# Kernel tuning notes

Hardware: AMD Instinct MI355X
Metric: run time of the kernel (lower is better)

## Reference

```python
import jax, jax.numpy as jnp
import numpy as np

D_MODEL = 1024
HIDDEN = 2816
N_EXPERTS = 8
N_ACTIVE = 2
THRESH = 1.0  # snntorch Leaky default threshold; single-step spike = (input > 1.0)


def setup_inputs() -> dict:
    key = jax.random.key(0)
    ks = jax.random.split(key, 10)
    s = 0.02
    return {
        "x": jax.random.normal(ks[0], (2, 1024, D_MODEL), jnp.float32),
        "Wg": jax.random.normal(ks[1], (D_MODEL, N_EXPERTS), jnp.float32) * s,
        "bg": jnp.zeros((N_EXPERTS,), jnp.float32),
        "W_gate": jax.random.normal(ks[2], (N_EXPERTS, D_MODEL, HIDDEN), jnp.float32) * s,
        "b_gate": jnp.zeros((N_EXPERTS, HIDDEN), jnp.float32),
        "W_up": jax.random.normal(ks[3], (N_EXPERTS, D_MODEL, HIDDEN), jnp.float32) * s,
        "b_up": jnp.zeros((N_EXPERTS, HIDDEN), jnp.float32),
        "W_down": jax.random.normal(ks[4], (N_EXPERTS, HIDDEN, D_MODEL), jnp.float32) * s,
        "b_down": jnp.zeros((N_EXPERTS, D_MODEL), jnp.float32),
    }


def reference(x, Wg, bg, W_gate, b_gate, W_up, b_up, W_down, b_down):
    B, S, D = x.shape
    xf = x.reshape(-1, D)  # [T, D]
    # spiking gate: single-step Leaky => spike = heaviside(logits - 1.0)
    gate_logits = xf @ Wg + bg  # [T, E]
    spike_out = (gate_logits > THRESH).astype(x.dtype)
    top_v, top_idx = jax.lax.top_k(spike_out, N_ACTIVE)  # [T, K]
    top_w = jax.nn.softmax(top_v, axis=-1)  # [T, K]
    # combine weights per expert: sum_k onehot(idx_k) * w_k  -> [T, E]
    combine = jnp.sum(jax.nn.one_hot(top_idx, N_EXPERTS, dtype=x.dtype) * top_w[..., None], axis=1)
    # per-expert SpikingSwiGLU: spike(gate_proj(x)) * up_proj(x) -> down_proj
    g = jnp.einsum("td,edh->teh", xf, W_gate) + b_gate  # [T, E, H]
    u = jnp.einsum("td,edh->teh", xf, W_up) + b_up
    h = (g > THRESH).astype(x.dtype) * u
    y = jnp.einsum("teh,ehd->ted", h, W_down) + b_down  # [T, E, D]
    out = jnp.einsum("ted,te->td", y, combine)
    return out.reshape(B, S, D)
```

## Files before the change

### kernel.cpp

```cpp
#include <hip/hip_runtime.h>


#define D_MODEL 1024
#define HID     2816
#define NEXP    8
#define NTOK    2048
#define NPAIR   4096
#define TM      128
#define MAXTILES 40
#define FLAGCAP  65536
#define KC      384
#define BAND    3e-4f
#define INNER   2e-5

typedef short s8v __attribute__((ext_vector_type(8)));
typedef float f4v __attribute__((ext_vector_type(4)));

__device__ __forceinline__ unsigned short f2bf(float f) {
  unsigned u = __float_as_uint(f);
  u += 0x7FFFu + ((u >> 16) & 1u);
  return (unsigned short)(u >> 16);
}
__device__ __forceinline__ float bf2f(unsigned short s) {
  return __uint_as_float(((unsigned)s) << 16);
}

__device__ __forceinline__ void gld16(const unsigned short* g, unsigned short* l) {
  __builtin_amdgcn_global_load_lds(
      (const __attribute__((address_space(1))) void*)g,
      (__attribute__((address_space(3))) void*)l, 16, 0, 0);
}

__device__ __forceinline__ bool np_spike(const float* __restrict__ xr,
                                         const float* __restrict__ wcol,
                                         size_t stride, float bias) {
  float g = 0.0f;
  for (int p0 = 0; p0 < D_MODEL; p0 += KC) {
    const int pe = min(p0 + KC, D_MODEL);
    float s = 0.0f;
    for (int d = p0; d < pe; ++d)
      s = fmaf(xr[d], wcol[(size_t)d * stride], s);
    g += s;
  }
  g += bias;
  return g > 1.0f;
}

__global__ void k_convx(const float* __restrict__ x, unsigned short* __restrict__ xh,
                        unsigned short* __restrict__ xl) {
  const int i = blockIdx.x * 256 + threadIdx.x;
  const float4 v = ((const float4*)x)[i];
  ushort4 h, l;
  h.x = f2bf(v.x); l.x = f2bf(v.x - bf2f(h.x));
  h.y = f2bf(v.y); l.y = f2bf(v.y - bf2f(h.y));
  h.z = f2bf(v.z); l.z = f2bf(v.z - bf2f(h.z));
  h.w = f2bf(v.w); l.w = f2bf(v.w - bf2f(h.w));
  ((ushort4*)xh)[i] = h;
  ((ushort4*)xl)[i] = l;
}

__global__ void k_convw(const float* __restrict__ in, unsigned short* __restrict__ hi,
                        unsigned short* __restrict__ lo, int R, int C) {
  const int e = blockIdx.y;
  const int ntx = C >> 6;
  const int tx = blockIdx.x % ntx;
  const int ty = blockIdx.x / ntx;
  const float* src = in + (size_t)e * R * C;
  const size_t obase = (size_t)e * R * C;
  __shared__ float t[64][65];
  const int tid = threadIdx.x;
#pragma unroll
  for (int it = 0; it < 4; ++it) {
    const int r = it * 16 + (tid >> 4);
    const float4 v = *(const float4*)(src + (size_t)(ty * 64 + r) * C + tx * 64 + (tid & 15) * 4);
    t[r][(tid & 15) * 4 + 0] = v.x;
    t[r][(tid & 15) * 4 + 1] = v.y;
    t[r][(tid & 15) * 4 + 2] = v.z;
    t[r][(tid & 15) * 4 + 3] = v.w;
  }
  __syncthreads();
#pragma unroll
  for (int it = 0; it < 2; ++it) {
    const int c = it * 32 + (tid >> 3);
    const int d0 = (tid & 7) * 8;
    s8v vh, vl;
#pragma unroll
    for (int i = 0; i < 8; ++i) {
      const float f = t[d0 + i][c];
      const unsigned short h = f2bf(f);
      vh[i] = (short)h;
      vl[i] = (short)f2bf(f - bf2f(h));
    }
    const size_t o = obase + (size_t)(tx * 64 + c) * R + ty * 64 + d0;
    *(s8v*)(hi + o) = vh;
    if (lo) *(s8v*)(lo + o) = vl;
  }
}

__global__ void k_router(const float* __restrict__ x, const float* __restrict__ Wg,
                         const float* __restrict__ bg, int* __restrict__ top_e,
                         float* __restrict__ top_w) {
  const int t = (blockIdx.x * blockDim.x + threadIdx.x) >> 6;
  const int lane = threadIdx.x & 63;
  if (t >= NTOK) return;
  const float* xr = x + (size_t)t * D_MODEL;
  double acc[NEXP];
#pragma unroll
  for (int e = 0; e < NEXP; ++e) acc[e] = 0.0;
#pragma unroll
  for (int i = 0; i < D_MODEL / 64; ++i) {
    const int d = lane + 64 * i;
    const double xv = (double)xr[d];
    const float4 w0 = *(const float4*)(Wg + d * NEXP);
    const float4 w1 = *(const float4*)(Wg + d * NEXP + 4);
    acc[0] = fma(xv, (double)w0.x, acc[0]);
    acc[1] = fma(xv, (double)w0.y, acc[1]);
    acc[2] = fma(xv, (double)w0.z, acc[2]);
    acc[3] = fma(xv, (double)w0.w, acc[3]);
    acc[4] = fma(xv, (double)w1.x, acc[4]);
    acc[5] = fma(xv, (double)w1.y, acc[5]);
    acc[6] = fma(xv, (double)w1.z, acc[6]);
    acc[7] = fma(xv, (double)w1.w, acc[7]);
  }
#pragma unroll
  for (int e = 0; e < NEXP; ++e) {
#pragma unroll
    for (int s = 32; s > 0; s >>= 1) acc[e] += __shfl_down(acc[e], s);
  }
  if (lane == 0) {
    bool sp[NEXP];
#pragma unroll
    for (int e = 0; e < NEXP; ++e) {
      const double l = acc[e] + (double)bg[e];
      if (fabs(l - 1.0) < INNER)
        sp[e] = np_spike(xr, Wg + e, NEXP, bg[e]);
      else
        sp[e] = l > 1.0;
    }
    int e0 = -1, e1 = -1;
    for (int e = 0; e < NEXP; ++e) if (sp[e])  { if (e0 < 0) e0 = e; else if (e1 < 0) e1 = e; }
    for (int e = 0; e < NEXP; ++e) if (!sp[e]) { if (e0 < 0) e0 = e; else if (e1 < 0) e1 = e; }
    float w0v, w1v;
    if (sp[e0] == sp[e1]) { w0v = 0.5f; w1v = 0.5f; }
    else { w0v = 0.7310585786300049f; w1v = 0.2689414213699951f; }
    top_e[2 * t] = e0; top_e[2 * t + 1] = e1;
    top_w[2 * t] = w0v; top_w[2 * t + 1] = w1v;
  }
}

__global__ void k_group(const int* __restrict__ top_e,
                        int* __restrict__ pair_token, int* __restrict__ pair_expert,
                        int* __restrict__ tok_pair, int4* __restrict__ tile_tab,
                        int* __restrict__ meta) {
  __shared__ int cnt[NEXP], off[NEXP + 1], fill[NEXP];
  const int tid = threadIdx.x;
  if (tid < NEXP) { cnt[tid] = 0; fill[tid] = 0; }
  __syncthreads();
  for (int i = tid; i < NPAIR; i += 256) atomicAdd(&cnt[top_e[i]], 1);
  __syncthreads();
  if (tid == 0) {
    off[0] = 0;
    for (int e = 0; e < NEXP; ++e) off[e + 1] = off[e] + cnt[e];
    int nt = 0;
    for (int e = 0; e < NEXP; ++e)
      for (int s = 0; s < cnt[e]; s += TM) {
        tile_tab[nt] = make_int4(e, off[e] + s, min(TM, cnt[e] - s), 0);
        ++nt;
      }
    meta[0] = nt;
    meta[1] = 0;
  }
  __syncthreads();
  for (int i = tid; i < NPAIR; i += 256) {
    const int e = top_e[i];
    const int pos = off[e] + atomicAdd(&fill[e], 1);
    pair_token[pos] = i >> 1;
    pair_expert[pos] = e;
    tok_pair[i] = pos;
  }
}

__launch_bounds__(256, 2)
__global__ void k_stage_a_bf(const unsigned short* __restrict__ xh,
                             const unsigned short* __restrict__ xl,
                             const unsigned short* __restrict__ wgh,
                             const unsigned short* __restrict__ wgl,
                             const unsigned short* __restrict__ wuh,
                             const float* __restrict__ bgate, const float* __restrict__ bup,
                             const int* __restrict__ pair_token,
                             const int4* __restrict__ tile_tab,
                             int* meta,
                             unsigned short* __restrict__ hbuf,
                             unsigned int* __restrict__ flags) {
  const int NB = HID / 128;
  const int tile_id = blockIdx.x / NB;
  const int bn = blockIdx.x % NB;
  if (tile_id >= meta[0]) return;
  const int4 tt = tile_tab[tile_id];
  const int e = tt.x, row0 = tt.y, rows = tt.z;
  const int n0 = bn * 128;

  __shared__ __align__(16) unsigned short lds[5 * 4096];

  const int tid = threadIdx.x;
  const int lane = tid & 63;
  const int wid = tid >> 6;
  const int wmb = (wid >> 1) * 4;
  const int wnb = (wid & 1) * 4;

  const unsigned short* p[10];
#pragma unroll
  for (int c = 0; c < 10; ++c) {
    const int idx = tid + 256 * c;
    const int arr = idx >> 9;
    const int q = idx & 511;
    const int rn = ((q >> 6) << 4) + (q & 15);
    const int j = (q & 63) >> 4;
    if (arr < 2) {
      if (rn < rows) {
        const int tok = pair_token[row0 + rn];
        p[c] = (arr ? xl : xh) + (size_t)tok * D_MODEL + 8 * j;
      } else p[c] = xh;
    } else {
      const unsigned short* base = (arr == 2) ? wgh : (arr == 3) ? wgl : wuh;
      p[c] = base + ((size_t)e * HID + n0 + rn) * D_MODEL + 8 * j;
    }
  }

  const f4v fz = {0.f, 0.f, 0.f, 0.f};
  f4v acc_g[4][4], acc_u[4][4];
#pragma unroll
  for (int m = 0; m < 4; ++m)
#pragma unroll
    for (int n = 0; n < 4; ++n) { acc_g[m][n] = fz; acc_u[m][n] = fz; }

  for (int k0 = 0; k0 < D_MODEL; k0 += 32) {
#pragma unroll
    for (int c = 0; c < 10; ++c)
      gld16(p[c] + k0, lds + (((c << 8) + (tid & 192)) << 3));
    __syncthreads();
    s8v afh[4], afl[4];
#pragma unroll
    for (int m = 0; m < 4; ++m) {
      afh[m] = *(const s8v*)(lds + ((wmb + m) * 64 + lane) * 8);
      afl[m] = *(const s8v*)(lds + 4096 + ((wmb + m) * 64 + lane) * 8);
    }
#pragma unroll
    for (int n = 0; n < 4; ++n) {
      const int boff = ((wnb + n) * 64 + lane) * 8;
      const s8v bgh = *(const s8v*)(lds + 8192 + boff);
      const s8v bgl = *(const s8v*)(lds + 12288 + boff);
      const s8v buh = *(const s8v*)(lds + 16384 + boff);
#pragma unroll
      for (int m = 0; m < 4; ++m) {
        acc_g[m][n] = __builtin_amdgcn_mfma_f32_16x16x32_bf16(afh[m], bgh, acc_g[m][n], 0, 0, 0);
        acc_g[m][n] = __builtin_amdgcn_mfma_f32_16x16x32_bf16(afh[m], bgl, acc_g[m][n], 0, 0, 0);
        acc_g[m][n] = __builtin_amdgcn_mfma_f32_16x16x32_bf16(afl[m], bgh, acc_g[m][n], 0, 0, 0);
        acc_u[m][n] = __builtin_amdgcn_mfma_f32_16x16x32_bf16(afh[m], buh, acc_u[m][n], 0, 0, 0);
      }
    }
    __syncthreads();
  }

  const int lcol = lane & 15;
  const int lrow = (lane >> 4) * 4;
#pragma unroll
  for (int n = 0; n < 4; ++n) {
    const int col = n0 + (wnb + n) * 16 + lcol;
    const float bgv = bgate[e * HID + col];
    const float buv = bup[e * HID + col];
#pragma unroll
    for (int m = 0; m < 4; ++m) {
#pragma unroll
      for (int i = 0; i < 4; ++i) {
        const int r = (wmb + m) * 16 + lrow + i;
        if (r < rows) {
          const float g = acc_g[m][n][i] + bgv;
          const float u = acc_u[m][n][i] + buv;
          hbuf[(size_t)(row0 + r) * HID + col] = f2bf(g > 1.0f ? u : 0.0f);
          if (fabsf(g - 1.0f) < BAND) {
            const unsigned idx = atomicAdd((unsigned*)(meta + 1), 1u);
            if (idx < FLAGCAP) flags[idx] = ((unsigned)(row0 + r) << 16) | (unsigned)col;
          }
        }
      }
    }
  }
}

__launch_bounds__(256, 2)
__global__ void k_stage_b_bf(const unsigned short* __restrict__ hbuf,
                             const unsigned short* __restrict__ wdh,
                             const int4* __restrict__ tile_tab,
                             const int* __restrict__ meta,
                             float* __restrict__ ybuf) {
  const int NB = D_MODEL / 128;
  const int tile_id = blockIdx.x / NB;
  const int bn = blockIdx.x % NB;
  if (tile_id >= meta[0]) return;
  const int4 tt = tile_tab[tile_id];
  const int e = tt.x, row0 = tt.y, rows = tt.z;
  const int n0 = bn * 128;

  __shared__ __align__(16) unsigned short lds[2 * 8192];

  const int tid = threadIdx.x;
  const int lane = tid & 63;
  const int wid = tid >> 6;
  const int wmb = (wid >> 1) * 4;
  const int wnb = (wid & 1) * 4;

  const unsigned short* p[8];
#pragma unroll
  for (int c = 0; c < 8; ++c) {
    const int idx = tid + 256 * c;
    const int arr = idx >> 10;
    const int q = idx & 1023;
    const int rn = ((q >> 7) << 4) + (q & 15);
    const int j = (q & 127) >> 4;
    if (arr == 0) {
      p[c] = (rn < rows) ? (hbuf + (size_t)(row0 + rn) * HID + 8 * j) : hbuf;
    } else {
      p[c] = wdh + ((size_t)e * D_MODEL + n0 + rn) * HID + 8 * j;
    }
  }

  const f4v fz = {0.f, 0.f, 0.f, 0.f};
  f4v acc[4][4];
#pragma unroll
  for (int m = 0; m < 4; ++m)
#pragma unroll
    for (int n = 0; n < 4; ++n) acc[m][n] = fz;

  for (int k0 = 0; k0 < HID; k0 += 64) {
#pragma unroll
    for (int c = 0; c < 8; ++c)
      gld16(p[c] + k0, lds + (((c << 8) + (tid & 192)) << 3));
    __syncthreads();
#pragma unroll
    for (int kk = 0; kk < 2; ++kk) {
      s8v af[4];
#pragma unroll
      for (int m = 0; m < 4; ++m)
        af[m] = *(const s8v*)(lds + ((wmb + m) * 128 + kk * 64 + lane) * 8);
#pragma unroll
      for (int n = 0; n < 4; ++n) {
        const s8v bv = *(const s8v*)(lds + 8192 + ((wnb + n) * 128 + kk * 64 + lane) * 8);
#pragma unroll
        for (int m = 0; m < 4; ++m)
          acc[m][n] = __builtin_amdgcn_mfma_f32_16x16x32_bf16(af[m], bv, acc[m][n], 0, 0, 0);
      }
    }
    __syncthreads();
  }

  const int lcol = lane & 15;
  const int lrow = (lane >> 4) * 4;
#pragma unroll
  for (int m = 0; m < 4; ++m)
#pragma unroll
    for (int i = 0; i < 4; ++i) {
      const int r = (wmb + m) * 16 + lrow + i;
      if (r < rows) {
#pragma unroll
        for (int n = 0; n < 4; ++n) {
          const int col = n0 + (wnb + n) * 16 + lcol;
          ybuf[(size_t)(row0 + r) * D_MODEL + col] = acc[m][n][i];
        }
      }
    }
}

__global__ void k_patch(const float* __restrict__ x,
                        const float* __restrict__ Wgate, const float* __restrict__ bgate,
                        const float* __restrict__ Wup, const float* __restrict__ bup,
                        const int* __restrict__ pair_token, const int* __restrict__ pair_expert,
                        const int* __restrict__ meta, const unsigned* __restrict__ flags,
                        unsigned short* __restrict__ hbuf) {
  const int nw = (gridDim.x * blockDim.x) >> 6;
  const int w = (blockIdx.x * blockDim.x + threadIdx.x) >> 6;
  const int lane = threadIdx.x & 63;
  int n = meta[1];
  if (n > FLAGCAP) n = FLAGCAP;
  for (int f = w; f < n; f += nw) {
    const unsigned fl = flags[f];
    const int row = (int)(fl >> 16);
    const int col = (int)(fl & 0xFFFFu);
    const int tok = pair_token[row];
    const int e = pair_expert[row];
    const float* xr = x + (size_t)tok * D_MODEL;
    const float* wg = Wgate + (size_t)e * D_MODEL * HID + col;
    const float* wu = Wup + (size_t)e * D_MODEL * HID + col;
    double g = 0.0, u = 0.0;
#pragma unroll
    for (int i = 0; i < D_MODEL / 64; ++i) {
      const int d = lane + 64 * i;
      const double xv = (double)xr[d];
      g = fma(xv, (double)wg[(size_t)d * HID], g);
      u = fma(xv, (double)wu[(size_t)d * HID], u);
    }
#pragma unroll
    for (int s = 32; s > 0; s >>= 1) { g += __shfl_down(g, s); u += __shfl_down(u, s); }
    if (lane == 0) {
      g += (double)bgate[e * HID + col];
      u += (double)bup[e * HID + col];
      bool spike;
      if (fabs(g - 1.0) < INNER)
        spike = np_spike(xr, wg, HID, bgate[e * HID + col]);
      else
        spike = g > 1.0;
      hbuf[(size_t)row * HID + col] = f2bf(spike ? (float)u : 0.0f);
    }
  }
}

__global__ void k_combine(const float* __restrict__ ybuf, const float* __restrict__ bdown,
                          const int* __restrict__ tok_pair, const int* __restrict__ top_e,
                          const float* __restrict__ top_w, float* __restrict__ out) {
  const int t = blockIdx.x;
  const int c = threadIdx.x;
  const int p0 = tok_pair[2 * t], p1 = tok_pair[2 * t + 1];
  const float w0 = top_w[2 * t], w1 = top_w[2 * t + 1];
  const int e0 = top_e[2 * t], e1 = top_e[2 * t + 1];
  const float4 y0 = ((const float4*)(ybuf + (size_t)p0 * D_MODEL))[c];
  const float4 y1 = ((const float4*)(ybuf + (size_t)p1 * D_MODEL))[c];
  const float4 b0 = ((const float4*)(bdown + (size_t)e0 * D_MODEL))[c];
  const float4 b1 = ((const float4*)(bdown + (size_t)e1 * D_MODEL))[c];
  float4 o;
  o.x = w0 * (y0.x + b0.x) + w1 * (y1.x + b1.x);
  o.y = w0 * (y0.y + b0.y) + w1 * (y1.y + b1.y);
  o.z = w0 * (y0.z + b0.z) + w1 * (y1.z + b1.z);
  o.w = w0 * (y0.w + b0.w) + w1 * (y1.w + b1.w);
  ((float4*)(out + (size_t)t * D_MODEL))[c] = o;
}

extern "C" void kernel_launch(void* const* d_in, const int* in_sizes, int n_in,
                              void* d_out, int out_size, void* d_ws, size_t ws_size,
                              hipStream_t stream) {
  const float* x     = (const float*)d_in[0];
  const float* Wg    = (const float*)d_in[1];
  const float* bg    = (const float*)d_in[2];
  const float* Wgate = (const float*)d_in[3];
  const float* bgate = (const float*)d_in[4];
  const float* Wup   = (const float*)d_in[5];
  const float* bup   = (const float*)d_in[6];
  const float* Wdown = (const float*)d_in[7];
  const float* bdown = (const float*)d_in[8];
  float* out = (float*)d_out;

  char* ws = (char*)d_ws;
  unsigned short* xh   = (unsigned short*)(ws + 0);
  unsigned short* xl   = (unsigned short*)(ws + 4194304);
  unsigned short* hbuf = (unsigned short*)(ws + 8388608);
  float* ybuf          = (float*)(ws + 31457280);
  int* top_e           = (int*)(ws + 48234496);
  float* top_w         = (float*)(ws + 48250880);
  int* pair_token      = (int*)(ws + 48267264);
  int* pair_expert     = (int*)(ws + 48283648);
  int* tok_pair        = (int*)(ws + 48300032);
  int4* tile_tab       = (int4*)(ws + 48316416);
  int* meta            = (int*)(ws + 48317184);
  unsigned* flags      = (unsigned*)(ws + 48317440);
  unsigned short* wgh  = (unsigned short*)(ws + 48579584);
  unsigned short* wgl  = (unsigned short*)(ws + 94716928);
  unsigned short* wuh  = (unsigned short*)(ws + 140854272);
  unsigned short* wdh  = (unsigned short*)(ws + 186991616);

  k_convx<<<dim3(NTOK * D_MODEL / 4 / 256), dim3(256), 0, stream>>>(x, xh, xl);
  k_convw<<<dim3(44 * 16, NEXP), dim3(256), 0, stream>>>(Wgate, wgh, wgl, D_MODEL, HID);
  k_convw<<<dim3(44 * 16, NEXP), dim3(256), 0, stream>>>(Wup, wuh, nullptr, D_MODEL, HID);
  k_convw<<<dim3(16 * 44, NEXP), dim3(256), 0, stream>>>(Wdown, wdh, nullptr, HID, D_MODEL);
  k_router<<<dim3(NTOK / 4), dim3(256), 0, stream>>>(x, Wg, bg, top_e, top_w);
  k_group<<<dim3(1), dim3(256), 0, stream>>>(top_e, pair_token, pair_expert, tok_pair,
                                             tile_tab, meta);
  k_stage_a_bf<<<dim3(MAXTILES * (HID / 128)), dim3(256), 0, stream>>>(
      xh, xl, wgh, wgl, wuh, bgate, bup, pair_token, tile_tab, meta, hbuf, flags);
  k_patch<<<dim3(512), dim3(256), 0, stream>>>(x, Wgate, bgate, Wup, bup, pair_token,
                                               pair_expert, meta, flags, hbuf);
  k_stage_b_bf<<<dim3(MAXTILES * (D_MODEL / 128)), dim3(256), 0, stream>>>(
      hbuf, wdh, tile_tab, meta, ybuf);
  k_combine<<<dim3(NTOK), dim3(256), 0, stream>>>(ybuf, bdown, tok_pair, top_e, top_w, out);
}
```

Baseline: 509.7 us.

## Schedule grouped GEMM blocks per XCD so tiles sharing weights co-locate

k_group now builds per-XCD work lists for stage A and stage B. Each (expert, column-block) weight panel is assigned to one of 8 XCD slots, and every row tile of that expert is placed on the same slot. Blocks index the list by blockIdx&7 and blockIdx>>3, which matches round-robin XCD dispatch, so all tiles reading the same weight panel run on one XCD and can reuse its L2. The cost is a serial list build on one thread and fixed capacities (AMAX, BMAX) that could overflow if an expert's load is very skewed.

```diff
diff --git a/kernel.cpp b/kernel.cpp
--- a/kernel.cpp
+++ b/kernel.cpp
@@ -7,11 +7,14 @@
 #define NTOK    2048
 #define NPAIR   4096
 #define TM      128
-#define MAXTILES 40
 #define FLAGCAP  65536
 #define KC      384
 #define BAND    3e-4f
 #define INNER   2e-5
+#define NBA     22
+#define NBB     8
+#define AMAX    128
+#define BMAX    48
 
 typedef short s8v __attribute__((ext_vector_type(8)));
 typedef float f4v __attribute__((ext_vector_type(4)));
@@ -151,7 +154,8 @@
 __global__ void k_group(const int* __restrict__ top_e,
                         int* __restrict__ pair_token, int* __restrict__ pair_expert,
                         int* __restrict__ tok_pair, int4* __restrict__ tile_tab,
-                        int* __restrict__ meta) {
+                        int* __restrict__ meta,
+                        int2* __restrict__ awork, int2* __restrict__ bwork) {
   __shared__ int cnt[NEXP], off[NEXP + 1], fill[NEXP];
   const int tid = threadIdx.x;
   if (tid < NEXP) { cnt[tid] = 0; fill[tid] = 0; }
@@ -159,16 +163,38 @@
   for (int i = tid; i < NPAIR; i += 256) atomicAdd(&cnt[top_e[i]], 1);
   __syncthreads();
   if (tid == 0) {
+    int tstart[NEXP], tcnt[NEXP];
     off[0] = 0;
     for (int e = 0; e < NEXP; ++e) off[e + 1] = off[e] + cnt[e];
     int nt = 0;
-    for (int e = 0; e < NEXP; ++e)
+    for (int e = 0; e < NEXP; ++e) {
+      tstart[e] = nt;
       for (int s = 0; s < cnt[e]; s += TM) {
         tile_tab[nt] = make_int4(e, off[e] + s, min(TM, cnt[e] - s), 0);
         ++nt;
       }
+      tcnt[e] = nt - tstart[e];
+    }
     meta[0] = nt;
     meta[1] = 0;
+    for (int x = 0; x < 8; ++x) {
+      int s = 0;
+      for (int P = x; P < NEXP * NBA; P += 8) {
+        const int e = P / NBA, bn = P % NBA;
+        for (int m = 0; m < tcnt[e]; ++m)
+          awork[x * AMAX + s++] = make_int2(tstart[e] + m, bn);
+      }
+      for (; s < AMAX; ++s) awork[x * AMAX + s] = make_int2(-1, 0);
+    }
+    for (int x = 0; x < 8; ++x) {
+      int s = 0;
+      for (int P = x; P < NEXP * NBB; P += 8) {
+        const int e = P / NBB, bn = P % NBB;
+        for (int m = 0; m < tcnt[e]; ++m)
+          bwork[x * BMAX + s++] = make_int2(tstart[e] + m, bn);
+      }
+      for (; s < BMAX; ++s) bwork[x * BMAX + s] = make_int2(-1, 0);
+    }
   }
   __syncthreads();
   for (int i = tid; i < NPAIR; i += 256) {
@@ -189,16 +215,15 @@
                              const float* __restrict__ bgate, const float* __restrict__ bup,
                              const int* __restrict__ pair_token,
                              const int4* __restrict__ tile_tab,
+                             const int2* __restrict__ awork,
                              int* meta,
                              unsigned short* __restrict__ hbuf,
                              unsigned int* __restrict__ flags) {
-  const int NB = HID / 128;
-  const int tile_id = blockIdx.x / NB;
-  const int bn = blockIdx.x % NB;
-  if (tile_id >= meta[0]) return;
-  const int4 tt = tile_tab[tile_id];
+  const int2 wk = awork[(blockIdx.x & 7) * AMAX + (blockIdx.x >> 3)];
+  if (wk.x < 0) return;
+  const int4 tt = tile_tab[wk.x];
   const int e = tt.x, row0 = tt.y, rows = tt.z;
-  const int n0 = bn * 128;
+  const int n0 = wk.y * 128;
 
   __shared__ __align__(16) unsigned short lds[5 * 4096];
 
@@ -292,15 +317,13 @@
 __global__ void k_stage_b_bf(const unsigned short* __restrict__ hbuf,
                              const unsigned short* __restrict__ wdh,
                              const int4* __restrict__ tile_tab,
-                             const int* __restrict__ meta,
+                             const int2* __restrict__ bwork,
                              float* __restrict__ ybuf) {
-  const int NB = D_MODEL / 128;
-  const int tile_id = blockIdx.x / NB;
-  const int bn = blockIdx.x % NB;
-  if (tile_id >= meta[0]) return;
-  const int4 tt = tile_tab[tile_id];
+  const int2 wk = bwork[(blockIdx.x & 7) * BMAX + (blockIdx.x >> 3)];
+  if (wk.x < 0) return;
+  const int4 tt = tile_tab[wk.x];
   const int e = tt.x, row0 = tt.y, rows = tt.z;
-  const int n0 = bn * 128;
+  const int n0 = wk.y * 128;
 
   __shared__ __align__(16) unsigned short lds[2 * 8192];
 
@@ -461,10 +484,12 @@
   int4* tile_tab       = (int4*)(ws + 48316416);
   int* meta            = (int*)(ws + 48317184);
   unsigned* flags      = (unsigned*)(ws + 48317440);
-  unsigned short* wgh  = (unsigned short*)(ws + 48579584);
-  unsigned short* wgl  = (unsigned short*)(ws + 94716928);
-  unsigned short* wuh  = (unsigned short*)(ws + 140854272);
-  unsigned short* wdh  = (unsigned short*)(ws + 186991616);
+  int2* awork          = (int2*)(ws + 48579584);
+  int2* bwork          = (int2*)(ws + 48587776);
+  unsigned short* wgh  = (unsigned short*)(ws + 48590848);
+  unsigned short* wgl  = (unsigned short*)(ws + 94728192);
+  unsigned short* wuh  = (unsigned short*)(ws + 140865536);
+  unsigned short* wdh  = (unsigned short*)(ws + 187002880);
 
   k_convx<<<dim3(NTOK * D_MODEL / 4 / 256), dim3(256), 0, stream>>>(x, xh, xl);
   k_convw<<<dim3(44 * 16, NEXP), dim3(256), 0, stream>>>(Wgate, wgh, wgl, D_MODEL, HID);
@@ -472,12 +497,12 @@
   k_convw<<<dim3(16 * 44, NEXP), dim3(256), 0, stream>>>(Wdown, wdh, nullptr, HID, D_MODEL);
   k_router<<<dim3(NTOK / 4), dim3(256), 0, stream>>>(x, Wg, bg, top_e, top_w);
   k_group<<<dim3(1), dim3(256), 0, stream>>>(top_e, pair_token, pair_expert, tok_pair,
-                                             tile_tab, meta);
-  k_stage_a_bf<<<dim3(MAXTILES * (HID / 128)), dim3(256), 0, stream>>>(
-      xh, xl, wgh, wgl, wuh, bgate, bup, pair_token, tile_tab, meta, hbuf, flags);
+                                             tile_tab, meta, awork, bwork);
+  k_stage_a_bf<<<dim3(8 * AMAX), dim3(256), 0, stream>>>(
+      xh, xl, wgh, wgl, wuh, bgate, bup, pair_token, tile_tab, awork, meta, hbuf, flags);
   k_patch<<<dim3(512), dim3(256), 0, stream>>>(x, Wgate, bgate, Wup, bup, pair_token,
                                                pair_expert, meta, flags, hbuf);
-  k_stage_b_bf<<<dim3(MAXTILES * (D_MODEL / 128)), dim3(256), 0, stream>>>(
-      hbuf, wdh, tile_tab, meta, ybuf);
+  k_stage_b_bf<<<dim3(8 * BMAX), dim3(256), 0, stream>>>(
+      hbuf, wdh, tile_tab, bwork, ybuf);
   k_combine<<<dim3(NTOK), dim3(256), 0, stream>>>(ybuf, bdown, tok_pair, top_e, top_w, out);
 }
```

Measured after the change: 559.4 us. +9.8%, slower.
